# Kernel optimization log

Hardware: AMD Instinct MI355X
Metric: run time of the kernel (lower is better)

The kernel has to match this reference:

```python
import jax, jax.numpy as jnp
import numpy as np

# Keras LSTM gate order: i, f, c(g), o; sigmoid recurrent activation, tanh activation.
# mask_zero=True semantics: at masked steps, h and c carry through unchanged and the
# emitted output equals the previous h (so return_sequences=False yields last valid h).

def _lstm(x, mask, W, U, b):
    # x: [B,S,D], mask: [B,S] bool, W: [D,4H], U: [H,4H], b: [4H]
    B, S, _ = x.shape
    H = U.shape[0]
    xz = jnp.einsum('bsd,dh->bsh', x, W) + b  # precompute input contributions
    h0 = jnp.zeros((B, H), x.dtype)
    c0 = jnp.zeros((B, H), x.dtype)
    def step(carry, inp):
        h, c = carry
        zx, m = inp  # zx: [B,4H], m: [B]
        z = zx + h @ U
        i, f, g, o = jnp.split(z, 4, axis=-1)
        c_new = jax.nn.sigmoid(f) * c + jax.nn.sigmoid(i) * jnp.tanh(g)
        h_new = jax.nn.sigmoid(o) * jnp.tanh(c_new)
        m = m[:, None]
        h = jnp.where(m, h_new, h)
        c = jnp.where(m, c_new, c)
        return (h, c), h
    (hT, _), hs = jax.lax.scan(step, (h0, c0), (jnp.swapaxes(xz, 0, 1), mask.T))
    return jnp.swapaxes(hs, 0, 1), hT  # [B,S,H], [B,H]


def _bilstm(x, mask, Wf, Uf, bf, Wb, Ub, bb, return_seq):
    hs_f, hT_f = _lstm(x, mask, Wf, Uf, bf)
    hs_b, hT_b = _lstm(x[:, ::-1], mask[:, ::-1], Wb, Ub, bb)
    if return_seq:
        return jnp.concatenate([hs_f, hs_b[:, ::-1]], axis=-1)
    return jnp.concatenate([hT_f, hT_b], axis=-1)


def _leaky(x):
    return jnp.where(x >= 0, x, 0.2 * x)  # tf.nn.leaky_relu alpha=0.2


def setup_inputs() -> dict:
    key = jax.random.key(0)
    ks = jax.random.split(key, 32)
    B, S, V, D, H = 64, 256, 32000, 300, 512
    s = 0.05
    inp = {}
    inp['text'] = jax.random.randint(ks[0], (B, S), 0, V)
    inp['emb'] = jax.random.normal(ks[1], (V, D), jnp.float32) * s
    # layer 0: input D, layer 1: input 2H
    inp['W0f'] = jax.random.normal(ks[2], (D, 4 * H), jnp.float32) * s
    inp['U0f'] = jax.random.normal(ks[3], (H, 4 * H), jnp.float32) * s
    inp['b0f'] = jnp.zeros((4 * H,), jnp.float32)
    inp['W0b'] = jax.random.normal(ks[4], (D, 4 * H), jnp.float32) * s
    inp['U0b'] = jax.random.normal(ks[5], (H, 4 * H), jnp.float32) * s
    inp['b0b'] = jnp.zeros((4 * H,), jnp.float32)
    inp['W1f'] = jax.random.normal(ks[6], (2 * H, 4 * H), jnp.float32) * s
    inp['U1f'] = jax.random.normal(ks[7], (H, 4 * H), jnp.float32) * s
    inp['b1f'] = jnp.zeros((4 * H,), jnp.float32)
    inp['W1b'] = jax.random.normal(ks[8], (2 * H, 4 * H), jnp.float32) * s
    inp['U1b'] = jax.random.normal(ks[9], (H, 4 * H), jnp.float32) * s
    inp['b1b'] = jnp.zeros((4 * H,), jnp.float32)
    inp['d0w'] = jax.random.normal(ks[10], (2 * H, 512), jnp.float32) * s
    inp['d0b'] = jnp.zeros((512,), jnp.float32)
    inp['d1w'] = jax.random.normal(ks[11], (512, 256), jnp.float32) * s
    inp['d1b'] = jnp.zeros((256,), jnp.float32)
    inp['d2w'] = jax.random.normal(ks[12], (256, 1), jnp.float32) * s
    inp['d2b'] = jnp.zeros((1,), jnp.float32)
    return inp


def reference(text, emb, W0f, U0f, b0f, W0b, U0b, b0b, W1f, U1f, b1f, W1b, U1b, b1b, d0w, d0b, d1w, d1b, d2w, d2b):
    mask = text != 0  # mask_zero=True
    x = emb[text]  # [B,S,D]
    x = _bilstm(x, mask, W0f, U0f, b0f, W0b, U0b, b0b, return_seq=True)  # [B,S,2H]
    # Dropout is identity at inference (training=False)
    x = _bilstm(x, mask, W1f, U1f, b1f, W1b, U1b, b1b, return_seq=False)  # [B,2H]
    x = _leaky(x @ d0w + d0b)
    x = _leaky(x @ d1w + d1b)
    out = x @ d2w + d2b  # [B,1]
    return out
```

## Files before the change

kernel.cpp:

```cpp
#include <hip/hip_runtime.h>
#include <hip/hip_fp16.h>
#include <math.h>

#define NB   64
#define NS   256
#define ND   300
#define NDP  320
#define NH   512
#define N4H  2048

typedef _Float16 half8_t __attribute__((ext_vector_type(8)));
typedef float    f32x4_t __attribute__((ext_vector_type(4)));

typedef const __attribute__((address_space(1))) unsigned int gas_u32;
typedef __attribute__((address_space(3))) unsigned int las_u32;

__device__ __forceinline__ float fast_sig(float x) {
  return 1.f / (1.f + __expf(-x));
}
__device__ __forceinline__ float fast_tanh(float x) {
  float ax = fabsf(x);
  float e  = __expf(2.f * ax);
  float r  = 1.f - 2.f / (e + 1.f);
  return copysignf(r, x);
}

__global__ void embed_f16_kernel(const int* __restrict__ text,
                                 const float* __restrict__ emb,
                                 _Float16* __restrict__ x) {
  int idx = blockIdx.x * 256 + threadIdx.x;
  const int total = NB * NS * NDP;
  for (; idx < total; idx += gridDim.x * 256) {
    int bs = idx / NDP;
    int d  = idx - bs * NDP;
    x[idx] = (d < ND) ? (_Float16)emb[(size_t)text[bs] * ND + d] : (_Float16)0.f;
  }
}

__global__ __launch_bounds__(256) void gemm_mfma_kernel(
    const _Float16* __restrict__ A, const float* __restrict__ W,
    const float* __restrict__ bias, __half* __restrict__ C,
    int M, int N, int K, int Kw) {
  __shared__ __align__(16) _Float16 as[128][40];
  __shared__ __align__(16) _Float16 ws16[128][40];
  __shared__ __align__(16) float    ws32[32][132];
  const int t = threadIdx.x;
  const int w = t >> 6;
  const int l = t & 63;
  const int lane16 = l & 15;
  const int kq = l >> 4;
  const int bm = blockIdx.y * 128;
  const int bn = blockIdx.x * 128;
  const int lr  = t >> 2;
  const int lsg = t & 3;
  const int wk  = t >> 3;
  const int wns = t & 7;
  const int rn  = t >> 1;
  const int rk0 = (t & 1) * 2;

  f32x4_t acc[2][8];
#pragma unroll
  for (int i = 0; i < 2; i++)
#pragma unroll
    for (int j = 0; j < 8; j++) acc[i][j] = (f32x4_t){0.f, 0.f, 0.f, 0.f};

  for (int k0 = 0; k0 < K; k0 += 32) {
#pragma unroll
    for (int h = 0; h < 2; h++) {
      int m = h * 64 + lr;
      *(uint4*)&as[m][lsg * 8] = *(const uint4*)(A + (size_t)(bm + m) * K + k0 + lsg * 8);
    }
    if (k0 + wk < Kw) {
#pragma unroll
      for (int i = 0; i < 4; i++)
        *(float4*)&ws32[wk][wns * 16 + i * 4] =
            *(const float4*)(W + (size_t)(k0 + wk) * N + bn + wns * 16 + i * 4);
    } else {
#pragma unroll
      for (int i = 0; i < 4; i++)
        *(float4*)&ws32[wk][wns * 16 + i * 4] = make_float4(0.f, 0.f, 0.f, 0.f);
    }
    __syncthreads();
#pragma unroll
    for (int g = 0; g < 2; g++) {
      int kqq = rk0 + g;
      half8_t hv;
#pragma unroll
      for (int jj = 0; jj < 8; jj++) hv[jj] = (_Float16)ws32[kqq * 8 + jj][rn];
      *(half8_t*)&ws16[rn][kqq * 8] = hv;
    }
    __syncthreads();
    half8_t afrag[2];
#pragma unroll
    for (int i = 0; i < 2; i++)
      afrag[i] = *(const half8_t*)&as[w * 32 + i * 16 + lane16][kq * 8];
#pragma unroll
    for (int j = 0; j < 8; j++) {
      half8_t bfrag = *(const half8_t*)&ws16[j * 16 + lane16][kq * 8];
#pragma unroll
      for (int i = 0; i < 2; i++)
        acc[i][j] = __builtin_amdgcn_mfma_f32_16x16x32_f16(afrag[i], bfrag, acc[i][j], 0, 0, 0);
    }
    __syncthreads();
  }
#pragma unroll
  for (int j = 0; j < 8; j++) {
    int col = bn + j * 16 + lane16;
    float bv = bias[col];
#pragma unroll
    for (int i = 0; i < 2; i++) {
      int rbase = bm + w * 32 + i * 16 + kq * 4;
#pragma unroll
      for (int r = 0; r < 4; r++)
        C[(size_t)(rbase + r) * N + col] = __float2half(acc[i][j][r] + bv);
    }
  }
}

__global__ __launch_bounds__(256, 1) void scan_ring_kernel(
    const __half* __restrict__ xzf, const __half* __restrict__ xzb,
    const float* __restrict__ Uf, const float* __restrict__ Ub,
    const int* __restrict__ text,
    __half* ring,
    int* flags, int* abortf,
    float* __restrict__ hT_out) {
  __shared__ __align__(16) _Float16 s_h[16 * 512];
  __shared__ __align__(16) float    s_z[4 * 16 * 20];

  const int t   = threadIdx.x;
  const int b   = blockIdx.x;
  const int grp = b & 7;
  const int dir = grp & 1;
  const int q16 = (grp >> 1) * 16;
  const int cblk = b >> 3;
  const int hc0  = cblk * 16;
  const __half* xz = dir ? xzb : xzf;
  const float* U = dir ? Ub : Uf;
  int* myflags = flags + grp * 32;

  const int w    = t >> 6;
  const int lane = t & 63;
  const int l16  = lane & 15;
  const int quad = lane >> 4;

  int st_off[4];
#pragma unroll
  for (int i = 0; i < 4; i++) {
    int qq = i * 256 + t;
    int lrow = qq >> 6, ch = qq & 63;
    st_off[i] = (q16 + lrow) * (NS * 1024) + ((ch ^ lrow) * 8);
  }
  const __half* ringd = ring + dir * NH;

  const int cc = t & 15, rr = t >> 4;
  const int gr = q16 + rr;
  int xz_off[4];
#pragma unroll
  for (int g = 0; g < 4; g++)
    xz_off[g] = gr * (NS * N4H) + g * NH + hc0 + cc;
  const int t_off = gr * NS;

  half8_t ufrag[16];
  {
    const int col = w * NH + hc0 + l16;
#pragma unroll
    for (int kt = 0; kt < 16; kt++)
#pragma unroll
      for (int jj = 0; jj < 8; jj++)
        ufrag[kt][jj] = (_Float16)U[(size_t)(kt * 32 + quad * 8 + jj) * N4H + col];
  }

  float c_st = 0.f, h_st = 0.f;
  __half xzr[4];
  int tmsk;
  {
    const int tt0 = dir ? (NS - 1) : 0;
#pragma unroll
    for (int g = 0; g < 4; g++) xzr[g] = xz[(size_t)tt0 * N4H + xz_off[g]];
    tmsk = text[t_off + tt0];
  }

  for (int s = 0; s < NS; s++) {
    const int tt = dir ? (NS - 1 - s) : s;
    f32x4_t acc = {0.f, 0.f, 0.f, 0.f};

    if (s > 0) {
      const int ttp = dir ? (tt + 1) : (tt - 1);
      const __half* srcb = ringd + (size_t)ttp * 1024;
#pragma unroll
      for (int i = 0; i < 4; i++)
        __builtin_amdgcn_global_load_lds((gas_u32*)(srcb + st_off[i]),
                                         (las_u32*)(s_h + (size_t)(i * 256 + t) * 8),
                                         16, 0, 0);
      __syncthreads();
#pragma unroll
      for (int kt = 0; kt < 16; kt++) {
        half8_t af = *(const half8_t*)(s_h + l16 * 512 + (((kt * 4 + quad)) ^ l16) * 8);
        acc = __builtin_amdgcn_mfma_f32_16x16x32_f16(af, ufrag[kt], acc, 0, 0, 0);
      }
    }

    *(f32x4_t*)&s_z[w * 320 + l16 * 20 + quad * 4] = acc;
    __syncthreads();

    {
      float zi = s_z[0 * 320 + cc * 20 + rr] + __half2float(xzr[0]);
      float zf = s_z[1 * 320 + cc * 20 + rr] + __half2float(xzr[1]);
      float zg = s_z[2 * 320 + cc * 20 + rr] + __half2float(xzr[2]);
      float zo = s_z[3 * 320 + cc * 20 + rr] + __half2float(xzr[3]);
      float ig = fast_sig(zi);
      float fg = fast_sig(zf);
      float gv = fast_tanh(zg);
      float og = fast_sig(zo);
      float cn = fg * c_st + ig * gv;
      float hn = og * fast_tanh(cn);
      if (tmsk != 0) { c_st = cn; h_st = hn; }
      ring[((size_t)gr * NS + tt) * 1024 + dir * NH + hc0 + cc] = __float2half(h_st);
      if (hT_out && s == NS - 1)
        hT_out[(size_t)gr * 1024 + dir * NH + hc0 + cc] = h_st;
    }

    if (s < NS - 1) {
      const int ttn = dir ? (tt - 1) : (tt + 1);
      __syncthreads();
      if (t == 0)
        __hip_atomic_store(myflags + cblk, s + 1, __ATOMIC_RELAXED,
                           __HIP_MEMORY_SCOPE_AGENT);
#pragma unroll
      for (int g = 0; g < 4; g++) xzr[g] = xz[(size_t)ttn * N4H + xz_off[g]];
      tmsk = text[t_off + ttn];
      {
        int aborted = 0, it = 0;
        while (true) {
          int f = __hip_atomic_load(myflags + (lane & 31),
                                    __ATOMIC_RELAXED, __HIP_MEMORY_SCOPE_AGENT);
          if (__all(f >= s + 1)) break;
          __builtin_amdgcn_s_sleep(2);
          if (((++it) & 1023) == 0) {
            if (it > 200000)
              __hip_atomic_store(abortf, 1, __ATOMIC_RELAXED, __HIP_MEMORY_SCOPE_AGENT);
            if (__hip_atomic_load(abortf, __ATOMIC_RELAXED, __HIP_MEMORY_SCOPE_AGENT)) {
              aborted = 1; break;
            }
          }
        }
        if (aborted) return;
      }
    }
  }
}

template <int ACT>
__global__ __launch_bounds__(256) void gemm_kernel(
    const float* __restrict__ A, const float* __restrict__ W,
    const float* __restrict__ bias, float* __restrict__ C,
    int M, int N, int K) {
  __shared__ __align__(16) float As[8][128];
  __shared__ __align__(16) float Bs[8][128];
  const int t  = threadIdx.x;
  const int bn = blockIdx.x * 128;
  const int bm = blockIdx.y * 128;
  const int tx = t & 15, ty = t >> 4;
  const int lm  = t >> 1;
  const int lk4 = (t & 1) * 4;
  const int lbk = t >> 5;
  const int lbn = (t & 31) * 4;
  float acc[8][8];
#pragma unroll
  for (int i = 0; i < 8; i++)
#pragma unroll
    for (int j = 0; j < 8; j++) acc[i][j] = 0.f;

  for (int k0 = 0; k0 < K; k0 += 8) {
#pragma unroll
    for (int i = 0; i < 4; i++) {
      int k = k0 + lk4 + i;
      int m = bm + lm;
      float v = 0.f;
      if (k < K && m < M) v = A[(size_t)m * K + k];
      As[lk4 + i][lm] = v;
    }
    {
      int k = k0 + lbk;
      float4 v = make_float4(0.f, 0.f, 0.f, 0.f);
      if (k < K) v = *(const float4*)(W + (size_t)k * N + bn + lbn);
      *(float4*)(&Bs[lbk][lbn]) = v;
    }
    __syncthreads();
#pragma unroll
    for (int kk = 0; kk < 8; kk++) {
      float a[8], bb[8];
      *(float4*)(a)      = *(const float4*)(&As[kk][ty * 8]);
      *(float4*)(a + 4)  = *(const float4*)(&As[kk][ty * 8 + 4]);
      *(float4*)(bb)     = *(const float4*)(&Bs[kk][tx * 8]);
      *(float4*)(bb + 4) = *(const float4*)(&Bs[kk][tx * 8 + 4]);
#pragma unroll
      for (int i = 0; i < 8; i++)
#pragma unroll
        for (int j = 0; j < 8; j++) acc[i][j] += a[i] * bb[j];
    }
    __syncthreads();
  }
  float4 bv0 = *(const float4*)(bias + bn + tx * 8);
  float4 bv1 = *(const float4*)(bias + bn + tx * 8 + 4);
#pragma unroll
  for (int i = 0; i < 8; i++) {
    int m = bm + ty * 8 + i;
    if (m >= M) continue;
    float4 o0, o1;
    o0.x = acc[i][0] + bv0.x; o0.y = acc[i][1] + bv0.y;
    o0.z = acc[i][2] + bv0.z; o0.w = acc[i][3] + bv0.w;
    o1.x = acc[i][4] + bv1.x; o1.y = acc[i][5] + bv1.y;
    o1.z = acc[i][6] + bv1.z; o1.w = acc[i][7] + bv1.w;
    if (ACT == 1) {
      o0.x = o0.x >= 0.f ? o0.x : 0.2f * o0.x;  o0.y = o0.y >= 0.f ? o0.y : 0.2f * o0.y;
      o0.z = o0.z >= 0.f ? o0.z : 0.2f * o0.z;  o0.w = o0.w >= 0.f ? o0.w : 0.2f * o0.w;
      o1.x = o1.x >= 0.f ? o1.x : 0.2f * o1.x;  o1.y = o1.y >= 0.f ? o1.y : 0.2f * o1.y;
      o1.z = o1.z >= 0.f ? o1.z : 0.2f * o1.z;  o1.w = o1.w >= 0.f ? o1.w : 0.2f * o1.w;
    }
    *(float4*)(C + (size_t)m * N + bn + tx * 8)     = o0;
    *(float4*)(C + (size_t)m * N + bn + tx * 8 + 4) = o1;
  }
}

__global__ void final_kernel(const float* __restrict__ a1, const float* __restrict__ w,
                             const float* __restrict__ bias, float* __restrict__ out) {
  const int b = blockIdx.x, t = threadIdx.x;
  float v = a1[b * 256 + t] * w[t];
#pragma unroll
  for (int off = 32; off > 0; off >>= 1) v += __shfl_down(v, off, 64);
  __shared__ float red[4];
  if ((t & 63) == 0) red[t >> 6] = v;
  __syncthreads();
  if (t == 0) out[b] = (red[0] + red[1]) + (red[2] + red[3]) + bias[0];
}

extern "C" void kernel_launch(void* const* d_in, const int* in_sizes, int n_in,
                              void* d_out, int out_size, void* d_ws, size_t ws_size,
                              hipStream_t stream) {
  const int*   text = (const int*)  d_in[0];
  const float* emb  = (const float*)d_in[1];
  const float* W0f  = (const float*)d_in[2];
  const float* U0f  = (const float*)d_in[3];
  const float* b0f  = (const float*)d_in[4];
  const float* W0b  = (const float*)d_in[5];
  const float* U0b  = (const float*)d_in[6];
  const float* b0b  = (const float*)d_in[7];
  const float* W1f  = (const float*)d_in[8];
  const float* U1f  = (const float*)d_in[9];
  const float* b1f  = (const float*)d_in[10];
  const float* W1b  = (const float*)d_in[11];
  const float* U1b  = (const float*)d_in[12];
  const float* b1b  = (const float*)d_in[13];
  const float* d0w  = (const float*)d_in[14];
  const float* d0b  = (const float*)d_in[15];
  const float* d1w  = (const float*)d_in[16];
  const float* d1b  = (const float*)d_in[17];
  const float* d2w  = (const float*)d_in[18];
  const float* d2b  = (const float*)d_in[19];
  float* out = (float*)d_out;

  char* p = (char*)d_ws;
  __half* xzA = (__half*)p;  p += (size_t)NB * NS * N4H * 2;
  __half* xzB = (__half*)p;  p += (size_t)NB * NS * N4H * 2;
  char* region1 = p;         p += (size_t)NB * NS * 1024 * 2;
  _Float16* x_emb = (_Float16*)region1;
  __half*   hs0   = (__half*)region1;
  __half* hp0  = (__half*)p;  p += 64 * 1024 * 2;
  __half* hp1  = (__half*)p;  p += 64 * 1024 * 2;
  int*    cnt  = (int*)p;     p += 64 * 1024 * 4;
  float*  feat = (float*)p;   p += 64 * 1024 * 4;
  float*  a0   = (float*)p;   p += 64 * 512 * 4;
  float*  a1   = (float*)p;   p += 64 * 256 * 4;
  (void)hp0; (void)hp1;
  int* flags0 = cnt;
  int* flags1 = cnt + 256;
  int* abortf = cnt + 512;

  hipMemsetAsync(cnt, 0, 516 * sizeof(int), stream);
  hipLaunchKernelGGL(embed_f16_kernel, dim3(4096), dim3(256), 0, stream, text, emb, x_emb);

  dim3 gmf(16, 128);
  hipLaunchKernelGGL(gemm_mfma_kernel, gmf, dim3(256), 0, stream, x_emb, W0f, b0f, xzA, 16384, N4H, NDP, ND);
  hipLaunchKernelGGL(gemm_mfma_kernel, gmf, dim3(256), 0, stream, x_emb, W0b, b0b, xzB, 16384, N4H, NDP, ND);

  hipLaunchKernelGGL(scan_ring_kernel, dim3(256), dim3(256), 0, stream,
                     xzA, xzB, U0f, U0b, text, hs0, flags0, abortf, (float*)nullptr);

  hipLaunchKernelGGL(gemm_mfma_kernel, gmf, dim3(256), 0, stream, (const _Float16*)hs0, W1f, b1f, xzA, 16384, N4H, 1024, 1024);
  hipLaunchKernelGGL(gemm_mfma_kernel, gmf, dim3(256), 0, stream, (const _Float16*)hs0, W1b, b1b, xzB, 16384, N4H, 1024, 1024);

  hipLaunchKernelGGL(scan_ring_kernel, dim3(256), dim3(256), 0, stream,
                     xzA, xzB, U1f, U1b, text, hs0, flags1, abortf, feat);

  gemm_kernel<1><<<dim3(4, 1), dim3(256), 0, stream>>>(feat, d0w, d0b, a0, 64, 512, 1024);
  gemm_kernel<1><<<dim3(2, 1), dim3(256), 0, stream>>>(a0, d1w, d1b, a1, 64, 256, 512);
  hipLaunchKernelGGL(final_kernel, dim3(64), dim3(256), 0, stream, a1, d2w, d2b, out);
}
```

Measured before the change: 2.366 ms.

## Rework embedding gather, GEMM tile loading, and double-buffer scan input prefetch

The embedding kernel now runs one block per token row, so the division and modulo per element go away. The input-projection GEMM loads its A tile straight into LDS with global_load_lds and an XOR swizzle. It also converts W to fp16 while reading it, which removes the fp32 staging buffer and one barrier. The recurrent scan keeps two sets of xz and mask registers so that values are prefetched two timesteps ahead, hiding global-load latency behind the inter-block wait. The per-column strided W reads may coalesce poorly compared with the earlier float4 row loads.

```diff
diff --git a/kernel.cpp b/kernel.cpp
--- a/kernel.cpp
+++ b/kernel.cpp
@@ -28,22 +28,20 @@
 __global__ void embed_f16_kernel(const int* __restrict__ text,
                                  const float* __restrict__ emb,
                                  _Float16* __restrict__ x) {
-  int idx = blockIdx.x * 256 + threadIdx.x;
-  const int total = NB * NS * NDP;
-  for (; idx < total; idx += gridDim.x * 256) {
-    int bs = idx / NDP;
-    int d  = idx - bs * NDP;
-    x[idx] = (d < ND) ? (_Float16)emb[(size_t)text[bs] * ND + d] : (_Float16)0.f;
-  }
+  const int bs = blockIdx.x;
+  const int tok = text[bs];
+  const float* src = emb + (size_t)tok * ND;
+  _Float16* dst = x + (size_t)bs * NDP;
+  for (int d = threadIdx.x; d < NDP; d += 256)
+    dst[d] = (d < ND) ? (_Float16)src[d] : (_Float16)0.f;
 }
 
 __global__ __launch_bounds__(256) void gemm_mfma_kernel(
     const _Float16* __restrict__ A, const float* __restrict__ W,
     const float* __restrict__ bias, __half* __restrict__ C,
     int M, int N, int K, int Kw) {
-  __shared__ __align__(16) _Float16 as[128][40];
-  __shared__ __align__(16) _Float16 ws16[128][40];
-  __shared__ __align__(16) float    ws32[32][132];
+  __shared__ __align__(16) _Float16 s_a[128 * 32];
+  __shared__ __align__(16) _Float16 s_w[128][40];
   const int t = threadIdx.x;
   const int w = t >> 6;
   const int l = t & 63;
@@ -51,12 +49,8 @@
   const int kq = l >> 4;
   const int bm = blockIdx.y * 128;
   const int bn = blockIdx.x * 128;
-  const int lr  = t >> 2;
-  const int lsg = t & 3;
-  const int wk  = t >> 3;
-  const int wns = t & 7;
-  const int rn  = t >> 1;
-  const int rk0 = (t & 1) * 2;
+  const int wcol = t >> 1;
+  const int wkh  = (t & 1) * 16;
 
   f32x4_t acc[2][8];
 #pragma unroll
@@ -66,37 +60,40 @@
 
   for (int k0 = 0; k0 < K; k0 += 32) {
 #pragma unroll
-    for (int h = 0; h < 2; h++) {
-      int m = h * 64 + lr;
-      *(uint4*)&as[m][lsg * 8] = *(const uint4*)(A + (size_t)(bm + m) * K + k0 + lsg * 8);
-    }
-    if (k0 + wk < Kw) {
-#pragma unroll
-      for (int i = 0; i < 4; i++)
-        *(float4*)&ws32[wk][wns * 16 + i * 4] =
-            *(const float4*)(W + (size_t)(k0 + wk) * N + bn + wns * 16 + i * 4);
-    } else {
-#pragma unroll
-      for (int i = 0; i < 4; i++)
-        *(float4*)&ws32[wk][wns * 16 + i * 4] = make_float4(0.f, 0.f, 0.f, 0.f);
-    }
-    __syncthreads();
-#pragma unroll
-    for (int g = 0; g < 2; g++) {
-      int kqq = rk0 + g;
-      half8_t hv;
-#pragma unroll
-      for (int jj = 0; jj < 8; jj++) hv[jj] = (_Float16)ws32[kqq * 8 + jj][rn];
-      *(half8_t*)&ws16[rn][kqq * 8] = hv;
+    for (int i = 0; i < 2; i++) {
+      int lchunk = i * 256 + t;
+      int row = lchunk >> 2;
+      int cq  = lchunk & 3;
+      int koff = (cq ^ ((row >> 1) & 3)) * 8;
+      __builtin_amdgcn_global_load_lds(
+          (gas_u32*)(A + (size_t)(bm + row) * K + k0 + koff),
+          (las_u32*)(s_a + (size_t)lchunk * 8), 16, 0, 0);
+    }
+    {
+      half8_t hv0, hv1;
+#pragma unroll
+      for (int jj = 0; jj < 8; jj++) {
+        int k = k0 + wkh + jj;
+        hv0[jj] = (k < Kw) ? (_Float16)W[(size_t)k * N + bn + wcol] : (_Float16)0.f;
+      }
+#pragma unroll
+      for (int jj = 0; jj < 8; jj++) {
+        int k = k0 + wkh + 8 + jj;
+        hv1[jj] = (k < Kw) ? (_Float16)W[(size_t)k * N + bn + wcol] : (_Float16)0.f;
+      }
+      *(half8_t*)&s_w[wcol][wkh]     = hv0;
+      *(half8_t*)&s_w[wcol][wkh + 8] = hv1;
     }
     __syncthreads();
     half8_t afrag[2];
 #pragma unroll
-    for (int i = 0; i < 2; i++)
-      afrag[i] = *(const half8_t*)&as[w * 32 + i * 16 + lane16][kq * 8];
+    for (int i = 0; i < 2; i++) {
+      int row = w * 32 + i * 16 + lane16;
+      afrag[i] = *(const half8_t*)(s_a + row * 32 + (kq ^ ((row >> 1) & 3)) * 8);
+    }
 #pragma unroll
     for (int j = 0; j < 8; j++) {
-      half8_t bfrag = *(const half8_t*)&ws16[j * 16 + lane16][kq * 8];
+      half8_t bfrag = *(const half8_t*)&s_w[j * 16 + lane16][kq * 8];
 #pragma unroll
       for (int i = 0; i < 2; i++)
         acc[i][j] = __builtin_amdgcn_mfma_f32_16x16x32_f16(afrag[i], bfrag, acc[i][j], 0, 0, 0);
@@ -171,13 +168,17 @@
   }
 
   float c_st = 0.f, h_st = 0.f;
-  __half xzr[4];
-  int tmsk;
+  __half xzrA[4], xzrB[4];
+  int tmA, tmB;
   {
-    const int tt0 = dir ? (NS - 1) : 0;
-#pragma unroll
-    for (int g = 0; g < 4; g++) xzr[g] = xz[(size_t)tt0 * N4H + xz_off[g]];
-    tmsk = text[t_off + tt0];
+    const int t0 = dir ? (NS - 1) : 0;
+    const int t1 = dir ? (NS - 2) : 1;
+#pragma unroll
+    for (int g = 0; g < 4; g++) xzrA[g] = xz[(size_t)t0 * N4H + xz_off[g]];
+    tmA = text[t_off + t0];
+#pragma unroll
+    for (int g = 0; g < 4; g++) xzrB[g] = xz[(size_t)t1 * N4H + xz_off[g]];
+    tmB = text[t_off + t1];
   }
 
   for (int s = 0; s < NS; s++) {
@@ -204,10 +205,13 @@
     __syncthreads();
 
     {
-      float zi = s_z[0 * 320 + cc * 20 + rr] + __half2float(xzr[0]);
-      float zf = s_z[1 * 320 + cc * 20 + rr] + __half2float(xzr[1]);
-      float zg = s_z[2 * 320 + cc * 20 + rr] + __half2float(xzr[2]);
-      float zo = s_z[3 * 320 + cc * 20 + rr] + __half2float(xzr[3]);
+      __half x0, x1, x2, x3; int tmsk;
+      if ((s & 1) == 0) { x0 = xzrA[0]; x1 = xzrA[1]; x2 = xzrA[2]; x3 = xzrA[3]; tmsk = tmA; }
+      else              { x0 = xzrB[0]; x1 = xzrB[1]; x2 = xzrB[2]; x3 = xzrB[3]; tmsk = tmB; }
+      float zi = s_z[0 * 320 + cc * 20 + rr] + __half2float(x0);
+      float zf = s_z[1 * 320 + cc * 20 + rr] + __half2float(x1);
+      float zg = s_z[2 * 320 + cc * 20 + rr] + __half2float(x2);
+      float zo = s_z[3 * 320 + cc * 20 + rr] + __half2float(x3);
       float ig = fast_sig(zi);
       float fg = fast_sig(zf);
       float gv = fast_tanh(zg);
@@ -221,14 +225,22 @@
     }
 
     if (s < NS - 1) {
-      const int ttn = dir ? (tt - 1) : (tt + 1);
       __syncthreads();
       if (t == 0)
         __hip_atomic_store(myflags + cblk, s + 1, __ATOMIC_RELAXED,
                            __HIP_MEMORY_SCOPE_AGENT);
-#pragma unroll
-      for (int g = 0; g < 4; g++) xzr[g] = xz[(size_t)ttn * N4H + xz_off[g]];
-      tmsk = text[t_off + ttn];
+      if (s + 2 < NS) {
+        const int tt2 = dir ? (tt - 2) : (tt + 2);
+        if ((s & 1) == 0) {
+#pragma unroll
+          for (int g = 0; g < 4; g++) xzrA[g] = xz[(size_t)tt2 * N4H + xz_off[g]];
+          tmA = text[t_off + tt2];
+        } else {
+#pragma unroll
+          for (int g = 0; g < 4; g++) xzrB[g] = xz[(size_t)tt2 * N4H + xz_off[g]];
+          tmB = text[t_off + tt2];
+        }
+      }
       {
         int aborted = 0, it = 0;
         while (true) {
@@ -378,7 +390,7 @@
   int* abortf = cnt + 512;
 
   hipMemsetAsync(cnt, 0, 516 * sizeof(int), stream);
-  hipLaunchKernelGGL(embed_f16_kernel, dim3(4096), dim3(256), 0, stream, text, emb, x_emb);
+  hipLaunchKernelGGL(embed_f16_kernel, dim3(NB * NS), dim3(256), 0, stream, text, emb, x_emb);
 
   dim3 gmf(16, 128);
   hipLaunchKernelGGL(gemm_mfma_kernel, gmf, dim3(256), 0, stream, x_emb, W0f, b0f, xzA, 16384, N4H, NDP, ND);
```

New measurement: 3.180 ms. 1.34x slower.
